# Kernel tuning notes

Hardware: AMD Instinct MI355X
Metric: run time of the kernel (lower is better)

Reference implementation:

```python
import jax, jax.numpy as jnp
import numpy as np

B, T, D_IN, D_OUT, H = 128, 128, 64, 64, 1024


def _lstm_cell(x_t, h, c, W_ih, W_hh, b_ih, b_hh):
    # PyTorch LSTMCell: gates = x@W_ih^T + b_ih + h@W_hh^T + b_hh, order [i, f, g, o]
    g = x_t @ W_ih.T + b_ih + h @ W_hh.T + b_hh  # [B, 4H]
    i, f, gg, o = jnp.split(g, 4, axis=-1)
    c_new = jax.nn.sigmoid(f) * c + jax.nn.sigmoid(i) * jnp.tanh(gg)
    h_new = jax.nn.sigmoid(o) * jnp.tanh(c_new)
    return h_new, c_new


def setup_inputs() -> dict:
    key = jax.random.key(0)
    ks = jax.random.split(key, 16)
    s_in = 1.0 / np.sqrt(H)
    inp = {
        "x": jax.random.normal(ks[0], (B, T, D_IN), dtype=jnp.float32),
        "W_ih1": jax.random.normal(ks[1], (4 * H, D_IN), dtype=jnp.float32) * s_in,
        "W_hh1": jax.random.normal(ks[2], (4 * H, H), dtype=jnp.float32) * s_in,
        "b_ih1": jax.random.normal(ks[3], (4 * H,), dtype=jnp.float32) * s_in,
        "b_hh1": jax.random.normal(ks[4], (4 * H,), dtype=jnp.float32) * s_in,
        "W_ih2": jax.random.normal(ks[5], (4 * H, H), dtype=jnp.float32) * s_in,
        "W_hh2": jax.random.normal(ks[6], (4 * H, H), dtype=jnp.float32) * s_in,
        "b_ih2": jax.random.normal(ks[7], (4 * H,), dtype=jnp.float32) * s_in,
        "b_hh2": jax.random.normal(ks[8], (4 * H,), dtype=jnp.float32) * s_in,
        "W_lin": jax.random.normal(ks[9], (D_IN, H), dtype=jnp.float32) * s_in,
        "b_lin": jax.random.normal(ks[10], (D_IN,), dtype=jnp.float32) * s_in,
        "W_hio": jax.random.normal(ks[11], (D_OUT, H), dtype=jnp.float32) * s_in,
        "b_hio": jax.random.normal(ks[12], (D_OUT,), dtype=jnp.float32) * s_in,
        "future": 1,
    }
    return inp


def reference(x, W_ih1, W_hh1, b_ih1, b_hh1, W_ih2, W_hh2, b_ih2, b_hh2,
              W_lin, b_lin, W_hio, b_hio, future):
    b = x.shape[0]
    h1 = jnp.zeros((b, H), x.dtype)
    c1 = jnp.zeros((b, H), x.dtype)
    h2 = jnp.zeros((b, H), x.dtype)
    c2 = jnp.zeros((b, H), x.dtype)

    def step(carry, x_t):
        h1, c1, h2, c2 = carry
        h1, c1 = _lstm_cell(x_t, h1, c1, W_ih1, W_hh1, b_ih1, b_hh1)
        h2, c2 = _lstm_cell(h1, h2, c2, W_ih2, W_hh2, b_ih2, b_hh2)
        return (h1, c1, h2, c2), None

    (h1, c1, h2, c2), _ = jax.lax.scan(step, (h1, c1, h2, c2),
                                       jnp.swapaxes(x, 0, 1))  # scan over T
    output = h2 @ W_lin.T + b_lin  # [B, D_IN] (only last step's value is used)

    for _ in range(int(future)):
        h1, c1 = _lstm_cell(output, h1, c1, W_ih1, W_hh1, b_ih1, b_hh1)
        h2, c2 = _lstm_cell(h1, h2, c2, W_ih2, W_hh2, b_ih2, b_hh2)
        output = h2 @ W_hio.T + b_hio  # [B, D_OUT]

    return output[:, None, :]  # [B, 1, D_OUT]
```

## Files before the change

### kernel.cpp

```cpp
#include <hip/hip_runtime.h>

#define B_   128
#define T_   128
#define DIN  64
#define H_   1024
#define NBLK 256
#define NTHR 1024

typedef _Float16 f16;
typedef _Float16 half8 __attribute__((ext_vector_type(8)));
typedef float float4v __attribute__((ext_vector_type(4)));
typedef unsigned uint2v __attribute__((ext_vector_type(2)));
typedef unsigned uint4v __attribute__((ext_vector_type(4)));


#define OFF_W2    34816
#define OFF_SG1A  100352
#define OFF_SG1B  109056
#define OFF_SG2A  117760
#define OFF_SG2B  126464
#define OFF_C1    135168
#define OFF_C2    137216
#define OFF_B1    139264
#define OFF_B2    139328
#define SMEM_BYTES 139392


struct Params {
  const float *x, *Wih1, *Whh1, *bih1, *bhh1, *Wih2, *Whh2, *bih2, *bhh2,
              *Wlin, *blin, *Whio, *bhio;
  const int* fut;
  float* out;
  f16 *x16, *h1a, *h1b, *h2a, *h2b, *ob;
  unsigned *arrive, *rel;
  unsigned *S;
};

__device__ __forceinline__ float sigm(float v) { return 1.f / (1.f + __expf(-v)); }
__device__ __forceinline__ float tanh_(float v) { return 2.f / (1.f + __expf(-2.f * v)) - 1.f; }

__device__ __forceinline__ unsigned get_xcc() {
  unsigned x;
  asm volatile("s_getreg_b32 %0, hwreg(HW_REG_XCC_ID)" : "=s"(x));
  return x & 15u;
}

__device__ __forceinline__ void grid_sync(unsigned* arrive, unsigned* rel, unsigned ph) {
  __syncthreads();
  const int tid = threadIdx.x, bid = blockIdx.x;
  if (bid == 0) {
    if (tid > 0 && tid < NBLK) {
      while (__hip_atomic_load(&arrive[tid], __ATOMIC_RELAXED, __HIP_MEMORY_SCOPE_AGENT) != ph)
        __builtin_amdgcn_s_sleep(8);
    }
    __syncthreads();
    if (tid == 0)
      __hip_atomic_store(rel, ph, __ATOMIC_RELEASE, __HIP_MEMORY_SCOPE_AGENT);
  } else {
    if (tid == 0) {
      __hip_atomic_store(&arrive[bid], ph, __ATOMIC_RELEASE, __HIP_MEMORY_SCOPE_AGENT);
      while (__hip_atomic_load(rel, __ATOMIC_RELAXED, __HIP_MEMORY_SCOPE_AGENT) != ph)
        __builtin_amdgcn_s_sleep(8);
    }
  }
  __syncthreads();
  __builtin_amdgcn_fence(__ATOMIC_ACQUIRE, "agent");
}

__device__ __forceinline__ void fast_sync(unsigned* S, unsigned x, unsigned xtotal,
                                          unsigned nxcd, unsigned ph) {
  __syncthreads();
  if (threadIdx.x == 0) {
    unsigned t = __hip_atomic_fetch_add(&S[x * 32], 1u, __ATOMIC_RELAXED, __HIP_MEMORY_SCOPE_AGENT);
    bool leader = (t % xtotal == 0u);
    if ((t + 1u) % xtotal == 0u) {
      unsigned c = __hip_atomic_fetch_add(&S[512], 1u, __ATOMIC_RELAXED, __HIP_MEMORY_SCOPE_AGENT);
      if ((c + 1u) % nxcd == 0u)
        __hip_atomic_store(&S[544], ph, __ATOMIC_RELAXED, __HIP_MEMORY_SCOPE_AGENT);
      asm volatile("buffer_inv sc0 sc1\n\ts_waitcnt vmcnt(0)" ::: "memory");
      __hip_atomic_store(&S[1088 + x * 32], ph, __ATOMIC_RELAXED, __HIP_MEMORY_SCOPE_AGENT);
    }
    if (leader) {
      while (__hip_atomic_load(&S[544], __ATOMIC_RELAXED, __HIP_MEMORY_SCOPE_AGENT) != ph)
        __builtin_amdgcn_s_sleep(1);
      while (__hip_atomic_load(&S[1088 + x * 32], __ATOMIC_RELAXED, __HIP_MEMORY_SCOPE_AGENT) != ph)
        __builtin_amdgcn_s_sleep(1);
      __hip_atomic_store(&S[576 + x * 32], ph, __ATOMIC_RELAXED, __HIP_MEMORY_SCOPE_AGENT);
      asm volatile("buffer_inv sc0\n\ts_waitcnt vmcnt(0)" ::: "memory");
    } else {
      while (__hip_atomic_load(&S[576 + x * 32], __ATOMIC_RELAXED, __HIP_MEMORY_SCOPE_AGENT) != ph)
        __builtin_amdgcn_s_sleep(2);
      asm volatile("buffer_inv sc0\n\ts_waitcnt vmcnt(0)" ::: "memory");
    }
  }
  __syncthreads();
}

__global__ void __launch_bounds__(NTHR, 4) lstm_k(Params p) {
  extern __shared__ char smem[];
  f16*   W1s  = (f16*)(smem);
  f16*   W2s  = (f16*)(smem + OFF_W2);
  float* Sg1A = (float*)(smem + OFF_SG1A);
  float* Sg1B = (float*)(smem + OFF_SG1B);
  float* Sg2A = (float*)(smem + OFF_SG2A);
  float* Sg2B = (float*)(smem + OFF_SG2B);
  float* c1   = (float*)(smem + OFF_C1);
  float* c2   = (float*)(smem + OFF_C2);
  float* bs1  = (float*)(smem + OFF_B1);
  float* bs2  = (float*)(smem + OFF_B2);

  const int tid = threadIdx.x, bid = blockIdx.x;
  const int hb  = bid * 4;
  const int fut = p.fut[0];
  const unsigned xcc = get_xcc();
  unsigned* S = p.S;

  if (bid == 0) {
    for (int i = tid; i < 2048; i += NTHR)
      __hip_atomic_store(&S[i], 0u, __ATOMIC_RELAXED, __HIP_MEMORY_SCOPE_AGENT);
  }

  for (int idx = tid; idx < 34 * 512; idx += NTHR) {
    int c = idx >> 9, r = idx & 511;
    int q = r >> 7, colw = (r >> 3) & 15, j = r & 7;
    int k = c * 32 + q * 8 + j;
    int row = (colw >> 2) * H_ + hb + (colw & 3);
    float v = (k < H_) ? p.Whh1[row * H_ + k] : p.Wih1[row * DIN + (k - H_)];
    W1s[idx] = (f16)v;
  }
  for (int idx = tid; idx < 64 * 512; idx += NTHR) {
    int c = idx >> 9, r = idx & 511;
    int q = r >> 7, colw = (r >> 3) & 15, j = r & 7;
    int k = c * 32 + q * 8 + j;
    int row = (colw >> 2) * H_ + hb + (colw & 3);
    float v = (k < H_) ? p.Wih2[row * H_ + k] : p.Whh2[row * H_ + (k - H_)];
    W2s[idx] = (f16)v;
  }
  if (tid < 16) {
    int row = (tid >> 2) * H_ + hb + (tid & 3);
    bs1[tid] = p.bih1[row] + p.bhh1[row];
    bs2[tid] = p.bih2[row] + p.bhh2[row];
  }
  for (int i = tid; i < 512; i += NTHR) { c1[i] = 0.f; c2[i] = 0.f; }
  for (int i = bid * NTHR + tid; i < B_ * T_ * DIN; i += NBLK * NTHR)
    p.x16[i] = (f16)p.x[i];
  for (int i = bid * NTHR + tid; i < B_ * H_; i += NBLK * NTHR) {
    p.h1a[i] = (f16)0.f; p.h1b[i] = (f16)0.f;
    p.h2a[i] = (f16)0.f; p.h2b[i] = (f16)0.f;
  }

  unsigned ph = 1;
  grid_sync(p.arrive, p.rel, ph);
  if (tid == 0)
    __hip_atomic_fetch_add(&S[1600 + xcc], 1u, __ATOMIC_RELAXED, __HIP_MEMORY_SCOPE_AGENT);
  ++ph;
  grid_sync(p.arrive, p.rel, ph);

  unsigned xtotal = __hip_atomic_load(&S[1600 + xcc], __ATOMIC_RELAXED, __HIP_MEMORY_SCOPE_AGENT);
  unsigned nxcd = 0;
  for (int i = 0; i < 16; ++i)
    nxcd += (__hip_atomic_load(&S[1600 + i], __ATOMIC_RELAXED, __HIP_MEMORY_SCOPE_AGENT) != 0u);

  auto gsync = [&]() { ++ph; fast_sync(S, xcc, xtotal, nxcd, ph); };

  const int lane = tid & 63, wq = tid >> 6;
  const int g  = wq >> 3;
  const int wv = wq & 7;
  const int col = lane & 15, quad = lane >> 4;
  const int m0 = wv * 16 + col;
  const int ko = quad * 8;
  const int jb = g * 16;
  const float b1v = g ? 0.f : bs1[col];
  const float b2v = g ? 0.f : bs2[col];
  const f16* W1f = W1s + lane * 8;
  const f16* W2f = W2s + lane * 8;
  float* S1w = g ? Sg1B : Sg1A;
  float* S2w = g ? Sg2B : Sg2A;
  const int hoff = quad * 1024 + m0 * 4;

  f16 *h1c = p.h1a, *h1n = p.h1b, *h2c = p.h2a, *h2n = p.h2b;

  auto lstm_pw = [&](const float* SgA, const float* SgB, float* cst, f16* hn) {
    int idx = tid & 511;
    int mm = idx >> 2, cc = idx & 3;
    int i0 = mm * 17 + cc;
    float gi = SgA[i0]      + SgB[i0];
    float gf = SgA[i0 + 4]  + SgB[i0 + 4];
    float gg = SgA[i0 + 8]  + SgB[i0 + 8];
    float go = SgA[i0 + 12] + SgB[i0 + 12];
    float cn = sigm(gf) * cst[idx] + sigm(gi) * tanh_(gg);
    cst[idx] = cn;
    f16 hv = (f16)(sigm(go) * tanh_(cn));
    int v = (int)__builtin_bit_cast(unsigned short, hv);
    int base = lane & ~3;
    int v0 = __shfl(v, base, 64),     v1 = __shfl(v, base + 1, 64);
    int v2 = __shfl(v, base + 2, 64), v3 = __shfl(v, base + 3, 64);
    if (cc == 0) {
      unsigned long long pk = (unsigned long long)(unsigned short)v0
        | ((unsigned long long)(unsigned short)v1 << 16)
        | ((unsigned long long)(unsigned short)v2 << 32)
        | ((unsigned long long)(unsigned short)v3 << 48);
      __hip_atomic_store((unsigned long long*)(hn + bid * 512 + mm * 4), pk,
                         __ATOMIC_RELAXED, __HIP_MEMORY_SCOPE_AGENT);
    }
  };

  auto ldwin = [&](const f16* hX, int j) -> half8 {
    const uint2v* q0 = (const uint2v*)(hX + j * 4096 + hoff);
    const uint2v* q1 = (const uint2v*)(hX + j * 4096 + hoff + 512);
    uint2v u0 = *q0, u1 = *q1;
    uint4v u = {u0[0], u0[1], u1[0], u1[1]};
    return __builtin_bit_cast(half8, u);
  };

  auto phase = [&](bool l1, bool l2, const f16* xp, int xstr) {
    float4v a1 = {b1v, b1v, b1v, b1v};
    float4v a2 = {b2v, b2v, b2v, b2v};

    if (l1) {
      half8 ax = *(const half8*)(xp + m0 * xstr + g * 32 + ko);
      a1 = __builtin_amdgcn_mfma_f32_16x16x32_f16(ax, *(const half8*)(W1f + (32 + g) * 512), a1, 0, 0, 0);
    }
    if (l1 && l2) {
      half8 pf1[4], pf2[4];
      #pragma unroll
      for (int i = 0; i < 4; ++i) { pf1[i] = ldwin(h1c, jb + i); pf2[i] = ldwin(h2c, jb + i); }
      #pragma unroll
      for (int i = 0; i < 16; ++i) {
        int j = jb + i;
        half8 w1 = pf1[i & 3];
        half8 w2 = pf2[i & 3];
        if (i < 12) { pf1[i & 3] = ldwin(h1c, jb + i + 4); pf2[i & 3] = ldwin(h2c, jb + i + 4); }
        a1 = __builtin_amdgcn_mfma_f32_16x16x32_f16(w1, *(const half8*)(W1f + j * 512), a1, 0, 0, 0);
        a2 = __builtin_amdgcn_mfma_f32_16x16x32_f16(w1, *(const half8*)(W2f + j * 512), a2, 0, 0, 0);
        a2 = __builtin_amdgcn_mfma_f32_16x16x32_f16(w2, *(const half8*)(W2f + (32 + j) * 512), a2, 0, 0, 0);
      }
    } else if (l1) {
      half8 pf1[8];
      #pragma unroll
      for (int i = 0; i < 8; ++i) pf1[i] = ldwin(h1c, jb + i);
      #pragma unroll
      for (int i = 0; i < 16; ++i) {
        int j = jb + i;
        half8 w1 = pf1[i & 7];
        if (i < 8) pf1[i & 7] = ldwin(h1c, jb + i + 8);
        a1 = __builtin_amdgcn_mfma_f32_16x16x32_f16(w1, *(const half8*)(W1f + j * 512), a1, 0, 0, 0);
      }
    } else if (l2) {
      half8 pf1[4], pf2[4];
      #pragma unroll
      for (int i = 0; i < 4; ++i) { pf1[i] = ldwin(h1c, jb + i); pf2[i] = ldwin(h2c, jb + i); }
      #pragma unroll
      for (int i = 0; i < 16; ++i) {
        int j = jb + i;
        half8 w1 = pf1[i & 3];
        half8 w2 = pf2[i & 3];
        if (i < 12) { pf1[i & 3] = ldwin(h1c, jb + i + 4); pf2[i & 3] = ldwin(h2c, jb + i + 4); }
        a2 = __builtin_amdgcn_mfma_f32_16x16x32_f16(w1, *(const half8*)(W2f + j * 512), a2, 0, 0, 0);
        a2 = __builtin_amdgcn_mfma_f32_16x16x32_f16(w2, *(const half8*)(W2f + (32 + j) * 512), a2, 0, 0, 0);
      }
    }

    __syncthreads();
    if (l1) {
      #pragma unroll
      for (int r = 0; r < 4; ++r)
        S1w[(wv * 16 + quad * 4 + r) * 17 + col] = a1[r];
    }
    if (l2) {
      #pragma unroll
      for (int r = 0; r < 4; ++r)
        S2w[(wv * 16 + quad * 4 + r) * 17 + col] = a2[r];
    }
    __syncthreads();
    if (tid < 512) {
      if (l1) lstm_pw(Sg1A, Sg1B, c1, h1n);
    } else {
      if (l2) lstm_pw(Sg2A, Sg2B, c2, h2n);
    }
  };

  auto out_phase = [&](const float* W, const float* bv, bool wout) {
    if (tid >= 512) return;
    int j = bid & 63, mgp = bid >> 6;
    int rid = tid >> 4, ks = tid & 15;
    int mrow = mgp * 32 + rid;
    const float* wr = W + j * H_ + ks * 64;
    float s = 0.f;
    #pragma unroll
    for (int q = 0; q < 16; ++q) {
      const uint2v* hp = (const uint2v*)(h2c + (ks * 16 + q) * 512 + mrow * 4);
      uint2v u = *hp;
      half8 hv4;
      { uint4v t = {u[0], u[1], 0u, 0u}; hv4 = __builtin_bit_cast(half8, t); }
      s += (float)hv4[0] * wr[q * 4 + 0] + (float)hv4[1] * wr[q * 4 + 1]
         + (float)hv4[2] * wr[q * 4 + 2] + (float)hv4[3] * wr[q * 4 + 3];
    }
    s += __shfl_down(s, 8, 16);
    s += __shfl_down(s, 4, 16);
    s += __shfl_down(s, 2, 16);
    s += __shfl_down(s, 1, 16);
    if (ks == 0) {
      float v = s + bv[j];
      f16 hv = (f16)v;
      __hip_atomic_store((unsigned short*)&p.ob[mrow * 64 + j],
                         __builtin_bit_cast(unsigned short, hv),
                         __ATOMIC_RELAXED, __HIP_MEMORY_SCOPE_AGENT);
      if (wout) p.out[mrow * 64 + j] = v;
    }
  };

  for (int t = -1; t < T_; ++t) {
    bool l1 = (t + 1 < T_), l2 = (t >= 0);
    phase(l1, l2, p.x16 + (t + 1) * DIN, T_ * DIN);
    gsync();
    if (l1) { f16* tm = h1c; h1c = h1n; h1n = tm; }
    if (l2) { f16* tm = h2c; h2c = h2n; h2n = tm; }
  }
  out_phase(p.Wlin, p.blin, fut == 0);
  gsync();
  for (int f = 0; f < fut; ++f) {
    phase(true, false, p.ob, 64);
    gsync();
    { f16* tm = h1c; h1c = h1n; h1n = tm; }
    phase(false, true, p.ob, 64);
    gsync();
    { f16* tm = h2c; h2c = h2n; h2n = tm; }
    out_phase(p.Whio, p.bhio, f == fut - 1);
    gsync();
  }
}

extern "C" void kernel_launch(void* const* d_in, const int* in_sizes, int n_in,
                              void* d_out, int out_size, void* d_ws, size_t ws_size,
                              hipStream_t stream) {
  char* w = (char*)d_ws;
  auto carve = [&](size_t n) { char* r = w; w += (n + 255) & ~(size_t)255; return r; };

  Params p;
  p.x    = (const float*)d_in[0];
  p.Wih1 = (const float*)d_in[1];
  p.Whh1 = (const float*)d_in[2];
  p.bih1 = (const float*)d_in[3];
  p.bhh1 = (const float*)d_in[4];
  p.Wih2 = (const float*)d_in[5];
  p.Whh2 = (const float*)d_in[6];
  p.bih2 = (const float*)d_in[7];
  p.bhh2 = (const float*)d_in[8];
  p.Wlin = (const float*)d_in[9];
  p.blin = (const float*)d_in[10];
  p.Whio = (const float*)d_in[11];
  p.bhio = (const float*)d_in[12];
  p.fut  = (const int*)d_in[13];
  p.out  = (float*)d_out;

  p.x16 = (f16*)carve((size_t)B_ * T_ * DIN * 2);
  p.h1a = (f16*)carve((size_t)B_ * H_ * 2);
  p.h1b = (f16*)carve((size_t)B_ * H_ * 2);
  p.h2a = (f16*)carve((size_t)B_ * H_ * 2);
  p.h2b = (f16*)carve((size_t)B_ * H_ * 2);
  p.ob  = (f16*)carve((size_t)B_ * 64 * 2);
  p.arrive = (unsigned*)carve(NBLK * sizeof(unsigned));
  p.rel    = (unsigned*)carve(256);
  p.S      = (unsigned*)carve(2048 * sizeof(unsigned));

  (void)hipFuncSetAttribute((const void*)lstm_k,
                            hipFuncAttributeMaxDynamicSharedMemorySize, SMEM_BYTES);
  void* args[] = { &p };
  (void)hipLaunchCooperativeKernel((void*)lstm_k, dim3(NBLK), dim3(NTHR),
                                   args, SMEM_BYTES, stream);
}
```

Before: 1.907 ms.

## Replace counter-based hierarchical grid barrier with per-block flags and XCD leader polling

Replaces the atomic-counter two-level barrier with a flag scheme. Each block writes its own arrival flag. One leader block per XCD polls all 256 flags in parallel, one thread per flag, then releases the other blocks on its XCD through a per-XCD flag. This removes contended fetch_add chains on shared counters from the per-step sync, at the cost of every XCD leader polling all block flags, which adds L2 and memory traffic.

```diff
diff --git a/kernel.cpp b/kernel.cpp
--- a/kernel.cpp
+++ b/kernel.cpp
@@ -67,29 +67,25 @@
   __builtin_amdgcn_fence(__ATOMIC_ACQUIRE, "agent");
 }
 
-__device__ __forceinline__ void fast_sync(unsigned* S, unsigned x, unsigned xtotal,
-                                          unsigned nxcd, unsigned ph) {
+__device__ __forceinline__ void fast_sync5(unsigned* S, unsigned x, bool lead, unsigned ph) {
   __syncthreads();
-  if (threadIdx.x == 0) {
-    unsigned t = __hip_atomic_fetch_add(&S[x * 32], 1u, __ATOMIC_RELAXED, __HIP_MEMORY_SCOPE_AGENT);
-    bool leader = (t % xtotal == 0u);
-    if ((t + 1u) % xtotal == 0u) {
-      unsigned c = __hip_atomic_fetch_add(&S[512], 1u, __ATOMIC_RELAXED, __HIP_MEMORY_SCOPE_AGENT);
-      if ((c + 1u) % nxcd == 0u)
-        __hip_atomic_store(&S[544], ph, __ATOMIC_RELAXED, __HIP_MEMORY_SCOPE_AGENT);
+  const int tid = threadIdx.x;
+  if (tid == 0)
+    __hip_atomic_store(&S[1664 + blockIdx.x], ph, __ATOMIC_RELEASE, __HIP_MEMORY_SCOPE_AGENT);
+  if (lead) {
+    if (tid < NBLK) {
+      while (__hip_atomic_load(&S[1664 + tid], __ATOMIC_RELAXED, __HIP_MEMORY_SCOPE_AGENT) != ph)
+        __builtin_amdgcn_s_sleep(1);
+    }
+    __syncthreads();
+    if (tid == 0) {
       asm volatile("buffer_inv sc0 sc1\n\ts_waitcnt vmcnt(0)" ::: "memory");
-      __hip_atomic_store(&S[1088 + x * 32], ph, __ATOMIC_RELAXED, __HIP_MEMORY_SCOPE_AGENT);
-    }
-    if (leader) {
-      while (__hip_atomic_load(&S[544], __ATOMIC_RELAXED, __HIP_MEMORY_SCOPE_AGENT) != ph)
+      __hip_atomic_store(&S[576 + x * 32], ph, __ATOMIC_RELAXED, __HIP_MEMORY_SCOPE_AGENT);
+    }
+  } else {
+    if (tid == 0) {
+      while (__hip_atomic_load(&S[576 + x * 32], __ATOMIC_RELAXED, __HIP_MEMORY_SCOPE_AGENT) != ph)
         __builtin_amdgcn_s_sleep(1);
-      while (__hip_atomic_load(&S[1088 + x * 32], __ATOMIC_RELAXED, __HIP_MEMORY_SCOPE_AGENT) != ph)
-        __builtin_amdgcn_s_sleep(1);
-      __hip_atomic_store(&S[576 + x * 32], ph, __ATOMIC_RELAXED, __HIP_MEMORY_SCOPE_AGENT);
-      asm volatile("buffer_inv sc0\n\ts_waitcnt vmcnt(0)" ::: "memory");
-    } else {
-      while (__hip_atomic_load(&S[576 + x * 32], __ATOMIC_RELAXED, __HIP_MEMORY_SCOPE_AGENT) != ph)
-        __builtin_amdgcn_s_sleep(2);
       asm volatile("buffer_inv sc0\n\ts_waitcnt vmcnt(0)" ::: "memory");
     }
   }
@@ -108,6 +104,7 @@
   float* c2   = (float*)(smem + OFF_C2);
   float* bs1  = (float*)(smem + OFF_B1);
   float* bs2  = (float*)(smem + OFF_B2);
+  __shared__ unsigned s_lead;
 
   const int tid = threadIdx.x, bid = blockIdx.x;
   const int hb  = bid * 4;
@@ -151,17 +148,16 @@
 
   unsigned ph = 1;
   grid_sync(p.arrive, p.rel, ph);
-  if (tid == 0)
-    __hip_atomic_fetch_add(&S[1600 + xcc], 1u, __ATOMIC_RELAXED, __HIP_MEMORY_SCOPE_AGENT);
+  if (tid == 0) {
+    unsigned old = __hip_atomic_fetch_add(&S[1600 + xcc], 1u, __ATOMIC_RELAXED, __HIP_MEMORY_SCOPE_AGENT);
+    s_lead = (old == 0u) ? 1u : 0u;
+  }
   ++ph;
   grid_sync(p.arrive, p.rel, ph);
 
-  unsigned xtotal = __hip_atomic_load(&S[1600 + xcc], __ATOMIC_RELAXED, __HIP_MEMORY_SCOPE_AGENT);
-  unsigned nxcd = 0;
-  for (int i = 0; i < 16; ++i)
-    nxcd += (__hip_atomic_load(&S[1600 + i], __ATOMIC_RELAXED, __HIP_MEMORY_SCOPE_AGENT) != 0u);
-
-  auto gsync = [&]() { ++ph; fast_sync(S, xcc, xtotal, nxcd, ph); };
+  const bool lead = (s_lead != 0u);
+
+  auto gsync = [&]() { ++ph; fast_sync5(S, xcc, lead, ph); };
 
   const int lane = tid & 63, wq = tid >> 6;
   const int g  = wq >> 3;
```

Measured after the change: 3.963 ms. 108% more time.
